# Kernel optimization log

Measured on AMD Instinct MI355X. Metric: run time of the kernel, lower is better.

Reference implementation:

```python
import jax, jax.numpy as jnp
import numpy as np


def _gelu(x):
    # torch.nn.functional.gelu default: exact erf form
    return jax.nn.gelu(x, approximate=False)


def setup_inputs() -> dict:
    key = jax.random.key(0)
    ks = jax.random.split(key, 6)
    B, L, H, MAXLEN = 8, 2048, 1024, 256
    former_input = jax.random.normal(ks[0], (B, L, H), dtype=jnp.float32)
    hidden_sates = jax.random.normal(ks[1], (B, L, H), dtype=jnp.float32)
    token_type_ids = jax.random.randint(ks[2], (B, L), 0, MAXLEN, dtype=jnp.int32)
    attention_mask = jnp.ones((B, L), dtype=jnp.float32)
    # learned params (init.normal_ std=0.02, biases zero)
    W_down = jax.random.normal(ks[3], (2 * H, H), dtype=jnp.float32) * 0.02
    b_down = jnp.zeros((H,), dtype=jnp.float32)
    W_row = jax.random.normal(ks[4], (H, H), dtype=jnp.float32) * 0.02
    b_row = jnp.zeros((H,), dtype=jnp.float32)
    return {
        "former_input": former_input,
        "hidden_sates": hidden_sates,
        "token_type_ids": token_type_ids,
        "attention_mask": attention_mask,
        "W_down": W_down,
        "b_down": b_down,
        "W_row": W_row,
        "b_row": b_row,
        "max_length": 256,
    }


def reference(former_input, hidden_sates, token_type_ids, attention_mask,
              W_down, b_down, W_row, b_row, max_length):
    # down_proj + gelu: [B, L, 2H] @ [2H, H] -> [B, L, H]
    x = jnp.concatenate([former_input, hidden_sates], axis=-1)
    sequence_output = _gelu(jnp.einsum("blf,fh->blh", x, W_down) + b_down)

    # one_hot_from @ sequence_output == segment-sum of tokens into table cells
    # cell_hidden[b, t] = sum_{l : token_type_ids[b,l]==t} sequence_output[b, l]
    seg = jax.vmap(lambda vals, ids: jax.ops.segment_sum(vals, ids, num_segments=max_length))
    cell_hidden = seg(sequence_output, token_type_ids)  # [B, max_length, H]

    # row_linear + gelu (dropout is identity in eval mode)
    cell_hidden = _gelu(jnp.einsum("bth,hk->btk", cell_hidden, W_row) + b_row)

    # one_hot_to @ cell_hidden == gather cell back to each token position
    seq_hidden = jnp.take_along_axis(
        cell_hidden, token_type_ids[:, :, None].astype(jnp.int32), axis=1
    )  # [B, L, H]
    return seq_hidden
```

## Files before the change

kernel.cpp:

```cpp
#include <hip/hip_runtime.h>

typedef unsigned short ushort_t;
typedef __bf16 bf16x8 __attribute__((ext_vector_type(8)));
typedef float f32x4 __attribute__((ext_vector_type(4)));

__device__ __forceinline__ unsigned short f2bf(float f) {
    unsigned u = __float_as_uint(f);
    u += 0x7fffu + ((u >> 16) & 1u);
    return (unsigned short)(u >> 16);
}
__device__ __forceinline__ float bf2f(unsigned short h) {
    return __uint_as_float(((unsigned)h) << 16);
}
__device__ __forceinline__ float gelu_f(float x) {
    return 0.5f * x * (1.0f + erff(x * 0.70710678118654752440f));
}

__global__ void convert_x_kernel(const float4* __restrict__ former,
                                 const float4* __restrict__ hidden,
                                 ushort4* __restrict__ Xb)
{
    int i = blockIdx.x * 256 + threadIdx.x;
    int row = i >> 9;
    int g = i & 511;
    float4 v = (g < 256) ? former[row * 256 + g] : hidden[row * 256 + (g - 256)];
    Xb[i] = make_ushort4(f2bf(v.x), f2bf(v.y), f2bf(v.z), f2bf(v.w));
}

__global__ void transpose_bf_kernel(const float* __restrict__ W, ushort_t* __restrict__ Wt,
                                    int R, int C)
{
    __shared__ float tile[32][33];
    const int bx = blockIdx.x * 32;
    const int by = blockIdx.y * 32;
    const int tx = threadIdx.x, ty = threadIdx.y;
    #pragma unroll
    for (int j = 0; j < 32; j += 8)
        tile[ty + j][tx] = W[(size_t)(by + ty + j) * C + bx + tx];
    __syncthreads();
    #pragma unroll
    for (int j = 0; j < 32; j += 8)
        Wt[(size_t)(bx + ty + j) * R + by + tx] = f2bf(tile[tx][ty + j]);
}

template <bool OUT_BF16>
__global__ void gemm_bias_gelu_kernel(const ushort_t* __restrict__ A,
                                      const ushort_t* __restrict__ Bt,
                                      const float* __restrict__ bias,
                                      void* __restrict__ C,
                                      int M, int N, int K)
{
    __shared__ __align__(16) ushort_t sA[128 * 64];
    __shared__ __align__(16) ushort_t sB[128 * 64];
    const int tid  = threadIdx.x;
    const int lane = tid & 63;
    const int wave = tid >> 6;
    const int wm = (wave & 1) * 64;
    const int wn = (wave >> 1) * 64;
    const long bm = (long)blockIdx.x * 128;
    const long bn = (long)blockIdx.y * 128;

    f32x4 acc[4][4] = {};

    const int srow = wave * 8 + (lane >> 3);
    const int scol = (lane & 7) * 8;
    const int ldsbase = wave * 512;

    for (int k0 = 0; k0 < K; k0 += 64) {
        __syncthreads();
        #pragma unroll
        for (int it = 0; it < 4; ++it) {
            const ushort_t* gA = A + (size_t)(bm + it * 32 + srow) * K + k0 + scol;
            const ushort_t* gB = Bt + (size_t)(bn + it * 32 + srow) * K + k0 + scol;
            __builtin_amdgcn_global_load_lds(
                (__attribute__((address_space(1))) void*)gA,
                (__attribute__((address_space(3))) void*)&sA[ldsbase + it * 2048], 16, 0, 0);
            __builtin_amdgcn_global_load_lds(
                (__attribute__((address_space(1))) void*)gB,
                (__attribute__((address_space(3))) void*)&sB[ldsbase + it * 2048], 16, 0, 0);
        }
        __syncthreads();

        const int arow = wm + (lane & 15);
        const int brow = wn + (lane & 15);
        const int kb = (lane >> 4) * 8;
        #pragma unroll
        for (int kk = 0; kk < 64; kk += 32) {
            bf16x8 af[4], bfr[4];
            #pragma unroll
            for (int t = 0; t < 4; ++t) {
                af[t]  = *(const bf16x8*)&sA[(arow + t * 16) * 64 + kk + kb];
                bfr[t] = *(const bf16x8*)&sB[(brow + t * 16) * 64 + kk + kb];
            }
            #pragma unroll
            for (int i = 0; i < 4; ++i)
                #pragma unroll
                for (int j = 0; j < 4; ++j)
                    acc[i][j] = __builtin_amdgcn_mfma_f32_16x16x32_bf16(af[i], bfr[j], acc[i][j], 0, 0, 0);
        }
    }

    #pragma unroll
    for (int i = 0; i < 4; ++i) {
        const long row0 = bm + wm + i * 16 + (lane >> 4) * 4;
        #pragma unroll
        for (int j = 0; j < 4; ++j) {
            const long col = bn + wn + j * 16 + (lane & 15);
            const float bv = bias[col];
            #pragma unroll
            for (int r = 0; r < 4; ++r) {
                float v = gelu_f(acc[i][j][r] + bv);
                if (OUT_BF16)
                    ((ushort_t*)C)[(size_t)(row0 + r) * N + col] = f2bf(v);
                else
                    ((float*)C)[(size_t)(row0 + r) * N + col] = v;
            }
        }
    }
}

__global__ void segsum_kernel(const ushort_t* __restrict__ seq,
                              const int* __restrict__ ids,
                              ushort_t* __restrict__ cell)
{
    const int b = blockIdx.x >> 8;
    const int t = blockIdx.x & 255;
    __shared__ int list[2048];
    __shared__ int count;
    if (threadIdx.x == 0) count = 0;
    __syncthreads();
    const int* idrow = ids + b * 2048;
    for (int l = threadIdx.x; l < 2048; l += 256) {
        if (idrow[l] == t) list[atomicAdd(&count, 1)] = l;
    }
    __syncthreads();
    const int n = count;
    float a0 = 0.f, a1 = 0.f, a2 = 0.f, a3 = 0.f;
    for (int i = 0; i < n; ++i) {
        const int l = list[i];
        const ushort4 v = *(const ushort4*)(seq + (size_t)(b * 2048 + l) * 1024 + threadIdx.x * 4);
        a0 += bf2f(v.x); a1 += bf2f(v.y); a2 += bf2f(v.z); a3 += bf2f(v.w);
    }
    ushort4* out = (ushort4*)(cell + (size_t)(b * 256 + t) * 1024);
    out[threadIdx.x] = make_ushort4(f2bf(a0), f2bf(a1), f2bf(a2), f2bf(a3));
}

__global__ void gather_kernel(const float4* __restrict__ cellout,
                              const int* __restrict__ ids,
                              float4* __restrict__ out)
{
    const int tok = blockIdx.x;
    const int b = tok >> 11;
    const int t = ids[tok];
    out[(size_t)tok * 256 + threadIdx.x] = cellout[(size_t)(b * 256 + t) * 256 + threadIdx.x];
}

extern "C" void kernel_launch(void* const* d_in, const int* in_sizes, int n_in,
                              void* d_out, int out_size, void* d_ws, size_t ws_size,
                              hipStream_t stream) {
    const float* former = (const float*)d_in[0];
    const float* hidden = (const float*)d_in[1];
    const int*   ids    = (const int*)d_in[2];
    const float* W_down = (const float*)d_in[4];
    const float* b_down = (const float*)d_in[5];
    const float* W_row  = (const float*)d_in[6];
    const float* b_row  = (const float*)d_in[7];
    float* out = (float*)d_out;

    char* ws = (char*)d_ws;
    ushort_t* Xb    = (ushort_t*)ws;  ws += (size_t)16384 * 2048 * 2;
    ushort_t* WdT   = (ushort_t*)ws;  ws += (size_t)1024 * 2048 * 2;
    ushort_t* WrT   = (ushort_t*)ws;  ws += (size_t)1024 * 1024 * 2;
    ushort_t* seq   = (ushort_t*)ws;  ws += (size_t)16384 * 1024 * 2;
    ushort_t* cellb = (ushort_t*)ws;  ws += (size_t)2048 * 1024 * 2;
    float*    cello = (float*)ws;

    convert_x_kernel<<<32768, 256, 0, stream>>>((const float4*)former, (const float4*)hidden,
                                                (ushort4*)Xb);
    transpose_bf_kernel<<<dim3(32, 64), dim3(32, 8), 0, stream>>>(W_down, WdT, 2048, 1024);
    transpose_bf_kernel<<<dim3(32, 32), dim3(32, 8), 0, stream>>>(W_row, WrT, 1024, 1024);

    gemm_bias_gelu_kernel<true><<<dim3(128, 8), 256, 0, stream>>>(Xb, WdT, b_down, seq,
                                                                  16384, 1024, 2048);
    segsum_kernel<<<2048, 256, 0, stream>>>(seq, ids, cellb);

    gemm_bias_gelu_kernel<false><<<dim3(16, 8), 256, 0, stream>>>(cellb, WrT, b_row, cello,
                                                                  2048, 1024, 1024);
    gather_kernel<<<16384, 256, 0, stream>>>((const float4*)cello, ids, (float4*)out);
}
```

Measured before the change: 327.9 us.

## Fuse input conversion and weight transposes into one prep kernel; swizzle GEMM LDS

Merges the X fp32→bf16 conversion and both weight transpose kernels into a single launch, with each thread now converting 8 elements using wider stores. Separately, the GEMM applies an XOR swizzle to the 16-byte column chunks in LDS, both when global_load_lds fills them and when the MFMA fragments are read. The swizzle is meant to remove LDS bank conflicts on the fragment reads, and the fused launch removes two kernel launches. The swizzle relies on the load and read index mappings staying consistent.

```diff
diff --git a/kernel.cpp b/kernel.cpp
--- a/kernel.cpp
+++ b/kernel.cpp
@@ -16,31 +16,42 @@
     return 0.5f * x * (1.0f + erff(x * 0.70710678118654752440f));
 }
 
-__global__ void convert_x_kernel(const float4* __restrict__ former,
-                                 const float4* __restrict__ hidden,
-                                 ushort4* __restrict__ Xb)
-{
-    int i = blockIdx.x * 256 + threadIdx.x;
-    int row = i >> 9;
-    int g = i & 511;
-    float4 v = (g < 256) ? former[row * 256 + g] : hidden[row * 256 + (g - 256)];
-    Xb[i] = make_ushort4(f2bf(v.x), f2bf(v.y), f2bf(v.z), f2bf(v.w));
-}
-
-__global__ void transpose_bf_kernel(const float* __restrict__ W, ushort_t* __restrict__ Wt,
-                                    int R, int C)
-{
-    __shared__ float tile[32][33];
-    const int bx = blockIdx.x * 32;
-    const int by = blockIdx.y * 32;
-    const int tx = threadIdx.x, ty = threadIdx.y;
-    #pragma unroll
-    for (int j = 0; j < 32; j += 8)
-        tile[ty + j][tx] = W[(size_t)(by + ty + j) * C + bx + tx];
-    __syncthreads();
-    #pragma unroll
-    for (int j = 0; j < 32; j += 8)
-        Wt[(size_t)(bx + ty + j) * R + by + tx] = f2bf(tile[tx][ty + j]);
+__global__ void prep_kernel(const float4* __restrict__ former,
+                            const float4* __restrict__ hidden,
+                            uint4* __restrict__ Xb4,
+                            const float* __restrict__ Wd, ushort_t* __restrict__ WdT,
+                            const float* __restrict__ Wr, ushort_t* __restrict__ WrT)
+{
+    const int blk = blockIdx.x;
+    const int tid = threadIdx.x;
+    if (blk < 16384) {
+        const int row = blk;
+        const float4* src = (tid < 128)
+            ? (former + (size_t)row * 256 + (tid & 127) * 2)
+            : (hidden + (size_t)row * 256 + (tid & 127) * 2);
+        float4 a = src[0], b = src[1];
+        uint4 o;
+        o.x = f2bf(a.x) | ((unsigned)f2bf(a.y) << 16);
+        o.y = f2bf(a.z) | ((unsigned)f2bf(a.w) << 16);
+        o.z = f2bf(b.x) | ((unsigned)f2bf(b.y) << 16);
+        o.w = f2bf(b.z) | ((unsigned)f2bf(b.w) << 16);
+        Xb4[(size_t)row * 256 + tid] = o;
+    } else {
+        __shared__ float tile[32][33];
+        const float* W; ushort_t* Wt; int R, C, b;
+        if (blk < 16384 + 2048) { b = blk - 16384; W = Wd; Wt = WdT; R = 2048; C = 1024; }
+        else                    { b = blk - 18432; W = Wr; Wt = WrT; R = 1024; C = 1024; }
+        const int bx = (b & 31) * 32;
+        const int by = (b >> 5) * 32;
+        const int tx = tid & 31, ty = tid >> 5;
+        #pragma unroll
+        for (int j = 0; j < 32; j += 8)
+            tile[ty + j][tx] = W[(size_t)(by + ty + j) * C + bx + tx];
+        __syncthreads();
+        #pragma unroll
+        for (int j = 0; j < 32; j += 8)
+            Wt[(size_t)(bx + ty + j) * R + by + tx] = f2bf(tile[tx][ty + j]);
+    }
 }
 
 template <bool OUT_BF16>
@@ -63,7 +74,7 @@
     f32x4 acc[4][4] = {};
 
     const int srow = wave * 8 + (lane >> 3);
-    const int scol = (lane & 7) * 8;
+    const int scol = ((lane & 7) ^ (lane >> 3)) * 8;
     const int ldsbase = wave * 512;
 
     for (int k0 = 0; k0 < K; k0 += 64) {
@@ -83,14 +94,16 @@
 
         const int arow = wm + (lane & 15);
         const int brow = wn + (lane & 15);
-        const int kb = (lane >> 4) * 8;
+        const int sw = lane & 7;
+        const int cbase = lane >> 4;
         #pragma unroll
         for (int kk = 0; kk < 64; kk += 32) {
+            const int koff = (((kk >> 3) + cbase) ^ sw) << 3;
             bf16x8 af[4], bfr[4];
             #pragma unroll
             for (int t = 0; t < 4; ++t) {
-                af[t]  = *(const bf16x8*)&sA[(arow + t * 16) * 64 + kk + kb];
-                bfr[t] = *(const bf16x8*)&sB[(brow + t * 16) * 64 + kk + kb];
+                af[t]  = *(const bf16x8*)&sA[(arow + t * 16) * 64 + koff];
+                bfr[t] = *(const bf16x8*)&sB[(brow + t * 16) * 64 + koff];
             }
             #pragma unroll
             for (int i = 0; i < 4; ++i)
@@ -175,10 +188,8 @@
     ushort_t* cellb = (ushort_t*)ws;  ws += (size_t)2048 * 1024 * 2;
     float*    cello = (float*)ws;
 
-    convert_x_kernel<<<32768, 256, 0, stream>>>((const float4*)former, (const float4*)hidden,
-                                                (ushort4*)Xb);
-    transpose_bf_kernel<<<dim3(32, 64), dim3(32, 8), 0, stream>>>(W_down, WdT, 2048, 1024);
-    transpose_bf_kernel<<<dim3(32, 32), dim3(32, 8), 0, stream>>>(W_row, WrT, 1024, 1024);
+    prep_kernel<<<19456, 256, 0, stream>>>((const float4*)former, (const float4*)hidden,
+                                           (uint4*)Xb, W_down, WdT, W_row, WrT);
 
     gemm_bias_gelu_kernel<true><<<dim3(128, 8), 256, 0, stream>>>(Xb, WdT, b_down, seq,
                                                                   16384, 1024, 2048);
```

Measured after the change: 318.1 us. 1.03x faster.
